# Kernel tuning notes

Measured on AMD Instinct MI355X. Metric: run time of the kernel, lower is better.

The kernel has to match this reference:

```python
import jax, jax.numpy as jnp
import numpy as np

N_NODES = 100000
N_EDGES = 1600000
D_IN = 128
D_HID = 128
D_OUT = 128
N_GRAPHS = 64


def setup_inputs() -> dict:
    key = jax.random.key(0)
    ks = jax.random.split(key, 10)
    x = jax.random.normal(ks[0], (N_NODES, D_IN), dtype=jnp.float32)
    edge_index = jax.random.randint(ks[1], (2, N_EDGES), 0, N_NODES, dtype=jnp.int64)
    graph_id = jnp.sort(jax.random.randint(ks[2], (N_NODES,), 0, N_GRAPHS, dtype=jnp.int64))
    s1 = 1.0 / np.sqrt(D_IN)
    s2 = 1.0 / np.sqrt(D_HID)
    s3 = 1.0 / np.sqrt(D_OUT)
    W1 = jax.random.normal(ks[3], (D_IN, D_HID), dtype=jnp.float32) * s1
    b1 = jnp.zeros((D_HID,), dtype=jnp.float32)
    W2 = jax.random.normal(ks[4], (D_HID, D_OUT), dtype=jnp.float32) * s2
    b2 = jnp.zeros((D_OUT,), dtype=jnp.float32)
    Wr1 = jax.random.normal(ks[5], (D_OUT, D_OUT), dtype=jnp.float32) * s3
    br1 = jnp.zeros((D_OUT,), dtype=jnp.float32)
    Wr2 = jax.random.normal(ks[6], (D_OUT, D_OUT), dtype=jnp.float32) * s3
    br2 = jnp.zeros((D_OUT,), dtype=jnp.float32)
    return {"x": x, "edge_index": edge_index, "graph_id": graph_id,
            "num_graphs": N_GRAPHS, "W1": W1, "b1": b1, "W2": W2, "b2": b2,
            "Wr1": Wr1, "br1": br1, "Wr2": Wr2, "br2": br2}


def _graph_conv(h, W, b, src, dst, norm_src, norm_dst, n_nodes):
    # DGL GraphConv, norm='both': out = D_dst^{-1/2} A (D_src^{-1/2} h) W + b
    h = h * norm_src[:, None]
    h = h @ W  # project first (cheap, keeps SpMM on the smaller/equal dim)
    agg = jax.ops.segment_sum(h[src], dst, num_segments=n_nodes)
    return agg * norm_dst[:, None] + b


def reference(x, edge_index, graph_id, num_graphs, W1, b1, W2, b2, Wr1, br1, Wr2, br2):
    src, dst = edge_index[0], edge_index[1]
    n_nodes = x.shape[0]
    ones = jnp.ones((src.shape[0],), dtype=x.dtype)
    deg_out = jax.ops.segment_sum(ones, src, num_segments=n_nodes)
    deg_in = jax.ops.segment_sum(ones, dst, num_segments=n_nodes)
    norm_src = jnp.clip(deg_out, 1.0) ** -0.5
    norm_dst = jnp.clip(deg_in, 1.0) ** -0.5

    # layer 1 + relu (dropout is identity in eval mode)
    h = _graph_conv(x, W1, b1, src, dst, norm_src, norm_dst, n_nodes)
    h = jax.nn.relu(h)
    # layer 2 + relu
    h = _graph_conv(h, W2, b2, src, dst, norm_src, norm_dst, n_nodes)
    h = jax.nn.relu(h)

    # per-graph mean pooling (dgl.mean_nodes)
    sums = jax.ops.segment_sum(h, graph_id, num_segments=num_graphs)
    counts = jax.ops.segment_sum(jnp.ones((n_nodes,), dtype=h.dtype), graph_id,
                                 num_segments=num_graphs)
    hg = sums / jnp.clip(counts, 1.0)[:, None]

    # readout MLP: Linear -> ReLU -> Linear
    out = jax.nn.relu(hg @ Wr1 + br1) @ Wr2 + br2
    return (out, h)
```

## Files before the change

### kernel.cpp

```cpp
#include <hip/hip_runtime.h>
#include <math.h>


#define D 128
#define BSH 8
#define BKT 256
#define CAP 4608
#define BGRID 1024

typedef _Float16 half8 __attribute__((ext_vector_type(8)));
typedef _Float16 half4v __attribute__((ext_vector_type(4)));
typedef _Float16 half2v __attribute__((ext_vector_type(2)));
typedef float f32x4 __attribute__((ext_vector_type(4)));

union H8 { half8 v; half2v h[4]; };

__global__ __launch_bounds__(256) void k_build(const int* __restrict__ src,
                                               const int* __restrict__ dst,
                                               int* __restrict__ cnt_d,
                                               int* __restrict__ cnt_s,
                                               int* __restrict__ packed_d,
                                               int* __restrict__ packed_s,
                                               const float* __restrict__ W1,
                                               const float* __restrict__ W2,
                                               _Float16* __restrict__ Wt1,
                                               _Float16* __restrict__ Wt2,
                                               const int* __restrict__ gid,
                                               int* __restrict__ gptr,
                                               int N, int E, int nbkt) {
  __shared__ int hd[512], hs[512], based[512], bases[512];
  const int t = threadIdx.x;
  const int bid = blockIdx.x;

  for (int idx = bid * 256 + t; idx < 2 * 128 * 128; idx += gridDim.x * 256) {
    int m = idx >> 14, i = idx & 16383;
    int k = i >> 7, n = i & 127;
    (m ? Wt2 : Wt1)[n * 128 + k] = (_Float16)((m ? W2 : W1)[i]);
  }
  if (bid == gridDim.x - 1 && t <= 64) {
    int lo = 0, hi = N;
    while (lo < hi) {
      int m = (lo + hi) >> 1;
      if (gid[m] < t) lo = m + 1; else hi = m;
    }
    gptr[t] = lo;
  }

  hd[t] = 0; hd[t + 256] = 0;
  hs[t] = 0; hs[t + 256] = 0;
  __syncthreads();
  int chunk = (E + gridDim.x - 1) / gridDim.x;
  int lo = bid * chunk, hi = min(lo + chunk, E);
  for (int i = lo + t; i < hi; i += 256) {
    atomicAdd(&hd[dst[i] >> BSH], 1);
    atomicAdd(&hs[src[i] >> BSH], 1);
  }
  __syncthreads();
  int c0d = hd[t], c1d = hd[t + 256];
  int c0s = hs[t], c1s = hs[t + 256];
  __syncthreads();
  hd[t] = 0; hd[t + 256] = 0;
  hs[t] = 0; hs[t + 256] = 0;
  if (t < nbkt)       based[t]       = c0d ? atomicAdd(&cnt_d[t], c0d) : 0;
  if (t + 256 < nbkt) based[t + 256] = c1d ? atomicAdd(&cnt_d[t + 256], c1d) : 0;
  if (t < nbkt)       bases[t]       = c0s ? atomicAdd(&cnt_s[t], c0s) : 0;
  if (t + 256 < nbkt) bases[t + 256] = c1s ? atomicAdd(&cnt_s[t + 256], c1s) : 0;
  __syncthreads();
  for (int i = lo + t; i < hi; i += 256) {
    int s = src[i], d = dst[i];
    int b1 = d >> BSH;
    int p1 = based[b1] + atomicAdd(&hd[b1], 1);
    if (p1 < CAP) packed_d[b1 * CAP + p1] = ((d & (BKT - 1)) << 17) | s;
    int b2 = s >> BSH;
    int p2 = bases[b2] + atomicAdd(&hs[b2], 1);
    if (p2 < CAP) packed_s[b2 * CAP + p2] = s & (BKT - 1);
  }
}

__global__ __launch_bounds__(512) void k_fine(const int* __restrict__ packed_d,
                                              const int* __restrict__ cnt_d,
                                              int* __restrict__ row_lo,
                                              int* __restrict__ row_hi,
                                              int* __restrict__ csr,
                                              const int* __restrict__ packed_s,
                                              const int* __restrict__ cnt_s,
                                              float* __restrict__ norm_src,
                                              int N, int nbkt) {
  __shared__ int hist[256];
  int t = threadIdx.x;
  if (blockIdx.x >= nbkt) {
    int b = blockIdx.x - nbkt;
    int lo = b * CAP;
    int cnt = min(cnt_s[b], CAP);
    if (t < 256) hist[t] = 0;
    __syncthreads();
    for (int e = t; e < cnt; e += 512)
      atomicAdd(&hist[packed_s[lo + e]], 1);
    __syncthreads();
    int nbase = b << BSH;
    if (t < 256 && nbase + t < N)
      norm_src[nbase + t] = rsqrtf(fmaxf((float)hist[t], 1.0f));
    return;
  }
  __shared__ int excl[256];
  __shared__ int ecache[CAP];
  __shared__ int sorted[CAP];
  int b = blockIdx.x;
  int lo = b * CAP;
  int cnt = min(cnt_d[b], CAP);
  if (t < 256) hist[t] = 0;
  __syncthreads();
  for (int e = t; e < cnt; e += 512) {
    int p = packed_d[lo + e];
    ecache[e] = p;
    atomicAdd(&hist[p >> 17], 1);
  }
  __syncthreads();
  int v = (t < 256) ? hist[t] : 0;
  for (int off = 1; off < 256; off <<= 1) {
    int a = (t >= off && t < 256) ? hist[t - off] : 0;
    __syncthreads();
    if (t < 256) hist[t] += a;
    __syncthreads();
  }
  int nbase = b << BSH;
  if (t < 256) {
    excl[t] = hist[t] - v;
    if (nbase + t < N) {
      row_lo[nbase + t] = lo + hist[t] - v;
      row_hi[nbase + t] = lo + hist[t];
    }
  }
  __syncthreads();
  if (t < 256) hist[t] = 0;
  __syncthreads();
  for (int e = t; e < cnt; e += 512) {
    int p = ecache[e];
    int dlow = p >> 17;
    int r = atomicAdd(&hist[dlow], 1);
    sorted[excl[dlow] + r] = p & 0x1FFFF;
  }
  __syncthreads();
  for (int e = t; e < cnt; e += 512)
    csr[lo + e] = sorted[e];
}

__global__ __launch_bounds__(256) void k_gemm1(const float* __restrict__ A,
                                               const _Float16* __restrict__ Wt,
                                               const float* __restrict__ scale,
                                               _Float16* __restrict__ C, int N) {
  __shared__ _Float16 As[64][136];
  __shared__ _Float16 Cs[64][128];
  const int r0 = blockIdx.x * 64;
  const int t = threadIdx.x;
  for (int i = t; i < 64 * 32; i += 256) {
    int r = i >> 5, c4 = i & 31;
    float4 v = {0.f, 0.f, 0.f, 0.f};
    if (r0 + r < N) {
      v = ((const float4*)A)[(size_t)(r0 + r) * 32 + c4];
      float s = scale[r0 + r];
      v.x *= s; v.y *= s; v.z *= s; v.w *= s;
    }
    half4v h = {(_Float16)v.x, (_Float16)v.y, (_Float16)v.z, (_Float16)v.w};
    *(half4v*)&As[r][c4 * 4] = h;
  }
  __syncthreads();
  const int w = t >> 6, l = t & 63;
  const int c = l & 15, quad = l >> 4;
  f32x4 acc[8];
#pragma unroll
  for (int nt = 0; nt < 8; ++nt) acc[nt] = (f32x4){0.f, 0.f, 0.f, 0.f};
#pragma unroll
  for (int kc = 0; kc < 4; ++kc) {
    half8 a = *(const half8*)&As[w * 16 + c][kc * 32 + quad * 8];
#pragma unroll
    for (int nt = 0; nt < 8; ++nt) {
      half8 b = *(const half8*)&Wt[(size_t)(nt * 16 + c) * 128 + kc * 32 + quad * 8];
      acc[nt] = __builtin_amdgcn_mfma_f32_16x16x32_f16(a, b, acc[nt], 0, 0, 0);
    }
  }
#pragma unroll
  for (int nt = 0; nt < 8; ++nt)
#pragma unroll
    for (int r = 0; r < 4; ++r)
      Cs[w * 16 + quad * 4 + r][nt * 16 + c] = (_Float16)acc[nt][r];
  __syncthreads();
  for (int i = t; i < 64 * 16; i += 256) {
    int r = i >> 4, c8 = i & 15;
    if (r0 + r < N)
      ((half8*)C)[(size_t)(r0 + r) * 16 + c8] = *(half8*)&Cs[r][c8 * 8];
  }
}

__global__ __launch_bounds__(256) void k_gemm2(const _Float16* __restrict__ A,
                                               const _Float16* __restrict__ Wt,
                                               _Float16* __restrict__ C, int N) {
  __shared__ _Float16 As[64][136];
  __shared__ _Float16 Cs[64][128];
  const int r0 = blockIdx.x * 64;
  const int t = threadIdx.x;
  for (int i = t; i < 64 * 16; i += 256) {
    int r = i >> 4, c8 = i & 15;
    half8 v = {0, 0, 0, 0, 0, 0, 0, 0};
    if (r0 + r < N) v = ((const half8*)A)[(size_t)(r0 + r) * 16 + c8];
    *(half8*)&As[r][c8 * 8] = v;
  }
  __syncthreads();
  const int w = t >> 6, l = t & 63;
  const int c = l & 15, quad = l >> 4;
  f32x4 acc[8];
#pragma unroll
  for (int nt = 0; nt < 8; ++nt) acc[nt] = (f32x4){0.f, 0.f, 0.f, 0.f};
#pragma unroll
  for (int kc = 0; kc < 4; ++kc) {
    half8 a = *(const half8*)&As[w * 16 + c][kc * 32 + quad * 8];
#pragma unroll
    for (int nt = 0; nt < 8; ++nt) {
      half8 b = *(const half8*)&Wt[(size_t)(nt * 16 + c) * 128 + kc * 32 + quad * 8];
      acc[nt] = __builtin_amdgcn_mfma_f32_16x16x32_f16(a, b, acc[nt], 0, 0, 0);
    }
  }
#pragma unroll
  for (int nt = 0; nt < 8; ++nt)
#pragma unroll
    for (int r = 0; r < 4; ++r)
      Cs[w * 16 + quad * 4 + r][nt * 16 + c] = (_Float16)acc[nt][r];
  __syncthreads();
  for (int i = t; i < 64 * 16; i += 256) {
    int r = i >> 4, c8 = i & 15;
    if (r0 + r < N)
      ((half8*)C)[(size_t)(r0 + r) * 16 + c8] = *(half8*)&Cs[r][c8 * 8];
  }
}

#define PK_ROW(u)                                                           \
  _Pragma("unroll")                                                         \
  for (int k = 0; k < 4; ++k) acch[k] += (u).h[k];

__device__ __forceinline__ void gather_core(const half8* __restrict__ P8,
                                            const int* __restrict__ csr,
                                            int start, int end, int cg, int eg,
                                            int lane, float* acc) {
  half2v acch[4] = {{(_Float16)0.f, (_Float16)0.f}, {(_Float16)0.f, (_Float16)0.f},
                    {(_Float16)0.f, (_Float16)0.f}, {(_Float16)0.f, (_Float16)0.f}};
  for (int s0 = start; s0 < end; s0 += 64) {
    int cnt = min(64, end - s0);
    int idx = (s0 + lane < end) ? csr[s0 + lane] : 0;
    int base = 0;
    for (; base + 16 <= cnt; base += 16) {
      int i0 = __shfl(idx, base + eg);
      int i1 = __shfl(idx, base + 4 + eg);
      int i2 = __shfl(idx, base + 8 + eg);
      int i3 = __shfl(idx, base + 12 + eg);
      H8 u0, u1, u2, u3;
      u0.v = P8[(size_t)i0 * 16 + cg];
      u1.v = P8[(size_t)i1 * 16 + cg];
      u2.v = P8[(size_t)i2 * 16 + cg];
      u3.v = P8[(size_t)i3 * 16 + cg];
      PK_ROW(u0) PK_ROW(u1) PK_ROW(u2) PK_ROW(u3)
    }
    for (; base + 4 <= cnt; base += 4) {
      int i0 = __shfl(idx, base + eg);
      H8 u0;
      u0.v = P8[(size_t)i0 * 16 + cg];
      PK_ROW(u0)
    }
    if (base < cnt) {
      int j = min(base + eg, cnt - 1);
      int i0 = __shfl(idx, j);
      if (base + eg < cnt) {
        H8 u0;
        u0.v = P8[(size_t)i0 * 16 + cg];
        PK_ROW(u0)
      }
    }
  }
#pragma unroll
  for (int k = 0; k < 4; ++k) {
    acc[2 * k]     = (float)acch[k].x;
    acc[2 * k + 1] = (float)acch[k].y;
  }
#pragma unroll
  for (int j = 0; j < 8; ++j) {
    acc[j] += __shfl_xor(acc[j], 16);
    acc[j] += __shfl_xor(acc[j], 32);
  }
}

__global__ __launch_bounds__(256) void k_gather1(const half8* __restrict__ P8,
                                                 const int* __restrict__ row_lo,
                                                 const int* __restrict__ row_hi,
                                                 const int* __restrict__ csr,
                                                 const float* __restrict__ bias,
                                                 const float* __restrict__ norm_src,
                                                 half2v* __restrict__ outH, int N) {
  int wid = (blockIdx.x * 256 + threadIdx.x) >> 6;
  if (wid >= N) return;
  int lane = threadIdx.x & 63;
  int cg = lane & 15, eg = lane >> 4;
  int start = row_lo[wid], end = row_hi[wid];
  float acc[8];
  gather_core(P8, csr, start, end, cg, eg, lane, acc);
  float nd = rsqrtf(fmaxf((float)(end - start), 1.0f));
  float ns = norm_src[wid];
  float2 b = ((const float2*)bias)[cg * 4 + eg];
  half2v o = {(_Float16)(fmaxf(acc[eg * 2] * nd + b.x, 0.f) * ns),
              (_Float16)(fmaxf(acc[eg * 2 + 1] * nd + b.y, 0.f) * ns)};
  outH[(size_t)wid * 64 + cg * 4 + eg] = o;
}

__global__ __launch_bounds__(256) void k_gather2(const half8* __restrict__ P8,
                                                 const int* __restrict__ row_lo,
                                                 const int* __restrict__ row_hi,
                                                 const int* __restrict__ csr,
                                                 const float* __restrict__ bias,
                                                 float2* __restrict__ outH, int N) {
  int wid = (blockIdx.x * 256 + threadIdx.x) >> 6;
  if (wid >= N) return;
  int lane = threadIdx.x & 63;
  int cg = lane & 15, eg = lane >> 4;
  int start = row_lo[wid], end = row_hi[wid];
  float acc[8];
  gather_core(P8, csr, start, end, cg, eg, lane, acc);
  float nd = rsqrtf(fmaxf((float)(end - start), 1.0f));
  float2 b = ((const float2*)bias)[cg * 4 + eg];
  float2 o;
  o.x = fmaxf(acc[eg * 2] * nd + b.x, 0.f);
  o.y = fmaxf(acc[eg * 2 + 1] * nd + b.y, 0.f);
  outH[(size_t)wid * 64 + cg * 4 + eg] = o;
}

__global__ __launch_bounds__(256) void k_pool(const float* __restrict__ H,
                                              const int* __restrict__ gptr,
                                              float* __restrict__ pool) {
  int g = blockIdx.x >> 3, chunk = blockIdx.x & 7;
  int col = threadIdx.x & 127, rpar = threadIdx.x >> 7;
  int s = gptr[g], e = gptr[g + 1];
  float acc = 0.0f;
  for (int r = s + chunk * 2 + rpar; r < e; r += 16)
    acc += H[(size_t)r * D + col];
  __shared__ float red[256];
  red[threadIdx.x] = acc;
  __syncthreads();
  if (rpar == 0) atomicAdd(&pool[g * D + col], acc + red[threadIdx.x + 128]);
}

__global__ __launch_bounds__(128) void k_readout(const float* __restrict__ pool,
                                                 const int* __restrict__ gptr,
                                                 const float* __restrict__ Wr1,
                                                 const float* __restrict__ br1,
                                                 const float* __restrict__ Wr2,
                                                 const float* __restrict__ br2,
                                                 float* __restrict__ out) {
  int g = blockIdx.x;
  int j = threadIdx.x;
  __shared__ float hg[D];
  __shared__ float t1[D];
  float cnt = fmaxf((float)(gptr[g + 1] - gptr[g]), 1.0f);
  hg[j] = pool[(size_t)g * D + j] / cnt;
  __syncthreads();
  float a = br1[j];
  for (int k = 0; k < D; ++k) a += hg[k] * Wr1[(size_t)k * D + j];
  t1[j] = fmaxf(a, 0.0f);
  __syncthreads();
  float b = br2[j];
  for (int k = 0; k < D; ++k) b += t1[k] * Wr2[(size_t)k * D + j];
  out[(size_t)g * D + j] = b;
}

extern "C" void kernel_launch(void* const* d_in, const int* in_sizes, int n_in,
                              void* d_out, int out_size, void* d_ws, size_t ws_size,
                              hipStream_t stream) {
  const float* x   = (const float*)d_in[0];
  const int* edge  = (const int*)d_in[1];
  const int* gid   = (const int*)d_in[2];
  const float* W1  = (const float*)d_in[4];
  const float* b1  = (const float*)d_in[5];
  const float* W2  = (const float*)d_in[6];
  const float* b2  = (const float*)d_in[7];
  const float* Wr1 = (const float*)d_in[8];
  const float* br1 = (const float*)d_in[9];
  const float* Wr2 = (const float*)d_in[10];
  const float* br2 = (const float*)d_in[11];

  const int N = in_sizes[0] / D;
  const int E = in_sizes[1] / 2;
  const int* src = edge;
  const int* dst = edge + E;
  const int nbkt = (N + BKT - 1) >> BSH;

  float* bufA     = (float*)d_ws;
  float* bufB     = bufA + (size_t)N * D;
  int* row_lo     = (int*)(bufB + (size_t)N * D);
  int* row_hi     = row_lo + N;
  int* csr        = row_hi + N;
  float* norm_src = (float*)(csr + (size_t)nbkt * CAP);
  float* pool     = norm_src + N;
  int* gptr       = (int*)(pool + 64 * D);
  int* cnt_d      = gptr + 65;
  int* cnt_s      = cnt_d + 512;
  _Float16* Wt1   = (_Float16*)(cnt_s + 512);
  _Float16* Wt2   = Wt1 + 128 * 128;
  int* packed_d   = (int*)bufA;
  int* packed_s   = packed_d + (size_t)nbkt * CAP;
  size_t need = ((size_t)2 * N * D + 3 * (size_t)N + (size_t)nbkt * CAP
                 + 64 * D + 65 + 1024 + 16384 + 1024) * sizeof(float);
  if (ws_size < need) return;

  float* out_g = (float*)d_out;
  float* h_out = out_g + 64 * D;

  _Float16* P   = (_Float16*)bufA;
  _Float16* h1p = (_Float16*)bufB;

  hipMemsetAsync(cnt_d, 0, 1024 * sizeof(int), stream);
  hipMemsetAsync(pool, 0, 64 * D * sizeof(float), stream);

  k_build<<<BGRID, 256, 0, stream>>>(src, dst, cnt_d, cnt_s, packed_d, packed_s,
                                     W1, W2, Wt1, Wt2, gid, gptr, N, E, nbkt);
  k_fine<<<2 * nbkt, 512, 0, stream>>>(packed_d, cnt_d, row_lo, row_hi, csr,
                                       packed_s, cnt_s, norm_src, N, nbkt);

  const int gemm_grid = (N + 63) / 64;

  k_gemm1<<<gemm_grid, 256, 0, stream>>>(x, Wt1, norm_src, P, N);
  k_gather1<<<(N * 64 + 255) / 256, 256, 0, stream>>>(
      (const half8*)P, row_lo, row_hi, csr, b1, norm_src, (half2v*)h1p, N);

  k_gemm2<<<gemm_grid, 256, 0, stream>>>(h1p, Wt2, P, N);
  k_gather2<<<(N * 64 + 255) / 256, 256, 0, stream>>>(
      (const half8*)P, row_lo, row_hi, csr, b2, (float2*)h_out, N);

  k_pool<<<64 * 8, 256, 0, stream>>>(h_out, gptr, pool);
  k_readout<<<64, 128, 0, stream>>>(pool, gptr, Wr1, br1, Wr2, br2, out_g);
}
```

Measured before the change: 418.7 us.

## Stage bucketed edges in shared memory and write coalesced runs per bucket

```diff
diff --git a/kernel.cpp b/kernel.cpp
--- a/kernel.cpp
+++ b/kernel.cpp
@@ -6,7 +6,7 @@
 #define BSH 8
 #define BKT 256
 #define CAP 4608
-#define BGRID 1024
+#define SCHUNK 3200
 
 typedef _Float16 half8 __attribute__((ext_vector_type(8)));
 typedef _Float16 half4v __attribute__((ext_vector_type(4)));
@@ -15,12 +15,12 @@
 
 union H8 { half8 v; half2v h[4]; };
 
-__global__ __launch_bounds__(256) void k_build(const int* __restrict__ src,
+__global__ __launch_bounds__(512) void k_build(const int* __restrict__ src,
                                                const int* __restrict__ dst,
                                                int* __restrict__ cnt_d,
                                                int* __restrict__ cnt_s,
                                                int* __restrict__ packed_d,
-                                               int* __restrict__ packed_s,
+                                               unsigned char* __restrict__ packed_s8,
                                                const float* __restrict__ W1,
                                                const float* __restrict__ W2,
                                                _Float16* __restrict__ Wt1,
@@ -28,11 +28,13 @@
                                                const int* __restrict__ gid,
                                                int* __restrict__ gptr,
                                                int N, int E, int nbkt) {
-  __shared__ int hd[512], hs[512], based[512], bases[512];
+  __shared__ int hd[512], hs[512], exd[512], exs[512], based[512], bases[512];
+  __shared__ int sd[SCHUNK];
+  __shared__ unsigned char ss[SCHUNK];
   const int t = threadIdx.x;
   const int bid = blockIdx.x;
 
-  for (int idx = bid * 256 + t; idx < 2 * 128 * 128; idx += gridDim.x * 256) {
+  for (int idx = bid * 512 + t; idx < 2 * 128 * 128; idx += gridDim.x * 512) {
     int m = idx >> 14, i = idx & 16383;
     int k = i >> 7, n = i & 127;
     (m ? Wt2 : Wt1)[n * 128 + k] = (_Float16)((m ? W2 : W1)[i]);
@@ -46,34 +48,58 @@
     gptr[t] = lo;
   }
 
-  hd[t] = 0; hd[t + 256] = 0;
-  hs[t] = 0; hs[t + 256] = 0;
-  __syncthreads();
-  int chunk = (E + gridDim.x - 1) / gridDim.x;
-  int lo = bid * chunk, hi = min(lo + chunk, E);
-  for (int i = lo + t; i < hi; i += 256) {
+  hd[t] = 0; hs[t] = 0;
+  __syncthreads();
+  const int chunk = (E + gridDim.x - 1) / gridDim.x;
+  const int lo = bid * chunk, hi = min(lo + chunk, E);
+  const int n = hi - lo;
+  for (int i = lo + t; i < hi; i += 512) {
     atomicAdd(&hd[dst[i] >> BSH], 1);
     atomicAdd(&hs[src[i] >> BSH], 1);
   }
   __syncthreads();
-  int c0d = hd[t], c1d = hd[t + 256];
-  int c0s = hs[t], c1s = hs[t + 256];
-  __syncthreads();
-  hd[t] = 0; hd[t + 256] = 0;
-  hs[t] = 0; hs[t + 256] = 0;
-  if (t < nbkt)       based[t]       = c0d ? atomicAdd(&cnt_d[t], c0d) : 0;
-  if (t + 256 < nbkt) based[t + 256] = c1d ? atomicAdd(&cnt_d[t + 256], c1d) : 0;
-  if (t < nbkt)       bases[t]       = c0s ? atomicAdd(&cnt_s[t], c0s) : 0;
-  if (t + 256 < nbkt) bases[t + 256] = c1s ? atomicAdd(&cnt_s[t + 256], c1s) : 0;
-  __syncthreads();
-  for (int i = lo + t; i < hi; i += 256) {
+  int cD = hd[t], cS = hs[t];
+  for (int off = 1; off < 512; off <<= 1) {
+    int ad = (t >= off) ? hd[t - off] : 0;
+    int as = (t >= off) ? hs[t - off] : 0;
+    __syncthreads();
+    hd[t] += ad; hs[t] += as;
+    __syncthreads();
+  }
+  exd[t] = hd[t] - cD;
+  exs[t] = hs[t] - cS;
+  if (t < nbkt) {
+    based[t] = cD ? atomicAdd(&cnt_d[t], cD) : 0;
+    bases[t] = cS ? atomicAdd(&cnt_s[t], cS) : 0;
+  }
+  __syncthreads();
+  hd[t] = 0; hs[t] = 0;
+  __syncthreads();
+  for (int i = lo + t; i < hi; i += 512) {
     int s = src[i], d = dst[i];
     int b1 = d >> BSH;
-    int p1 = based[b1] + atomicAdd(&hd[b1], 1);
-    if (p1 < CAP) packed_d[b1 * CAP + p1] = ((d & (BKT - 1)) << 17) | s;
+    int r1 = atomicAdd(&hd[b1], 1);
+    sd[exd[b1] + r1] = ((d & (BKT - 1)) << 17) | s;
     int b2 = s >> BSH;
-    int p2 = bases[b2] + atomicAdd(&hs[b2], 1);
-    if (p2 < CAP) packed_s[b2 * CAP + p2] = s & (BKT - 1);
+    int r2 = atomicAdd(&hs[b2], 1);
+    ss[exs[b2] + r2] = (unsigned char)(s & (BKT - 1));
+  }
+  __syncthreads();
+  for (int i = t; i < n; i += 512) {
+    int blo = 0, bhi = nbkt - 1;
+    while (blo < bhi) {
+      int m = (blo + bhi + 1) >> 1;
+      if (exd[m] <= i) blo = m; else bhi = m - 1;
+    }
+    int p = based[blo] + (i - exd[blo]);
+    if (p < CAP) packed_d[blo * CAP + p] = sd[i];
+    blo = 0; bhi = nbkt - 1;
+    while (blo < bhi) {
+      int m = (blo + bhi + 1) >> 1;
+      if (exs[m] <= i) blo = m; else bhi = m - 1;
+    }
+    p = bases[blo] + (i - exs[blo]);
+    if (p < CAP) packed_s8[blo * CAP + p] = ss[i];
   }
 }
 
@@ -82,7 +108,7 @@
                                               int* __restrict__ row_lo,
                                               int* __restrict__ row_hi,
                                               int* __restrict__ csr,
-                                              const int* __restrict__ packed_s,
+                                              const unsigned char* __restrict__ packed_s8,
                                               const int* __restrict__ cnt_s,
                                               float* __restrict__ norm_src,
                                               int N, int nbkt) {
@@ -90,12 +116,12 @@
   int t = threadIdx.x;
   if (blockIdx.x >= nbkt) {
     int b = blockIdx.x - nbkt;
-    int lo = b * CAP;
+    size_t lo = (size_t)b * CAP;
     int cnt = min(cnt_s[b], CAP);
     if (t < 256) hist[t] = 0;
     __syncthreads();
     for (int e = t; e < cnt; e += 512)
-      atomicAdd(&hist[packed_s[lo + e]], 1);
+      atomicAdd(&hist[packed_s8[lo + e]], 1);
     __syncthreads();
     int nbase = b << BSH;
     if (t < 256 && nbase + t < N)
@@ -402,7 +428,7 @@
   _Float16* Wt1   = (_Float16*)(cnt_s + 512);
   _Float16* Wt2   = Wt1 + 128 * 128;
   int* packed_d   = (int*)bufA;
-  int* packed_s   = packed_d + (size_t)nbkt * CAP;
+  unsigned char* packed_s8 = (unsigned char*)(packed_d + (size_t)nbkt * CAP);
   size_t need = ((size_t)2 * N * D + 3 * (size_t)N + (size_t)nbkt * CAP
                  + 64 * D + 65 + 1024 + 16384 + 1024) * sizeof(float);
   if (ws_size < need) return;
@@ -413,13 +439,15 @@
   _Float16* P   = (_Float16*)bufA;
   _Float16* h1p = (_Float16*)bufB;
 
-  hipMemsetAsync(cnt_d, 0, 1024 * sizeof(int), stream);
-  hipMemsetAsync(pool, 0, 64 * D * sizeof(float), stream);
-
-  k_build<<<BGRID, 256, 0, stream>>>(src, dst, cnt_d, cnt_s, packed_d, packed_s,
-                                     W1, W2, Wt1, Wt2, gid, gptr, N, E, nbkt);
+  hipMemsetAsync(pool, 0, (64 * D + 65 + 1024) * sizeof(float), stream);
+
+  const int build_grid = (E + SCHUNK - 1) / SCHUNK;
+  k_build<<<build_grid, 512, 0, stream>>>(src, dst, cnt_d, cnt_s,
+                                          packed_d, packed_s8,
+                                          W1, W2, Wt1, Wt2, gid, gptr,
+                                          N, E, nbkt);
   k_fine<<<2 * nbkt, 512, 0, stream>>>(packed_d, cnt_d, row_lo, row_hi, csr,
-                                       packed_s, cnt_s, norm_src, N, nbkt);
+                                       packed_s8, cnt_s, norm_src, N, nbkt);
 
   const int gemm_grid = (N + 63) / 64;
 
```

New measurement: 381.2 us. 8.9% less time.
